# Performance work log

Measured on AMD Instinct MI355X. Metric: run time of the kernel, lower is better.

The kernel has to match this reference:

```python
import jax, jax.numpy as jnp
from jax import lax
import numpy as np

WR = 7    # window resolution
NH = 4    # attention heads
FF = 3.0  # focusing factor


def _conv_bn(x, w, s, b, groups=1):
    # Conv2d (no bias) + inference BatchNorm folded to per-channel scale/bias
    y = lax.conv_general_dilated(x, w, (1, 1), 'SAME',
        dimension_numbers=('NCHW', 'OIHW', 'NCHW'), feature_group_count=groups)
    return y * s[None, :, None, None] + b[None, :, None, None]


def _ffn(x, w1, s1, b1, w2, s2, b2):
    return _conv_bn(jax.nn.relu(_conv_bn(x, w1, s1, b1)), w2, s2, b2)


def _focus(t):
    n0 = jnp.linalg.norm(t, axis=-1, keepdims=True)
    tp = t ** FF
    return tp / jnp.linalg.norm(tp, axis=-1, keepdims=True) * n0


def _attn(xw, wq, wkv, pos, scale_p, dwc_w, dwc_b, proj_w, proj_b):
    # xw: [Bw, N=49, C] focused linear attention within one window
    Bw, N, C = xw.shape
    hd = C // NH
    q = xw @ wq.T
    kv = xw @ wkv.T
    k, v = kv[..., :C], kv[..., C:]
    k = k + pos
    sc = jax.nn.softplus(scale_p)
    q = (jax.nn.relu(q) + 1e-6) / sc
    k = (jax.nn.relu(k) + 1e-6) / sc
    q, k = _focus(q), _focus(k)
    heads = lambda t: t.reshape(Bw, N, NH, hd).transpose(0, 2, 1, 3).reshape(Bw * NH, N, hd)
    q, k, v = heads(q), heads(k), heads(v)
    z = 1.0 / (jnp.einsum('bic,bc->bi', q, k.sum(axis=1)) + 1e-6)
    # static cost-based path choice (matches torch: i=j=N, c=d=hd)
    if N * N * (hd + hd) > hd * hd * (N + N):
        kv2 = jnp.einsum('bjc,bjd->bcd', k, v)
        y = jnp.einsum('bic,bcd,bi->bid', q, kv2, z)
    else:
        qk = jnp.einsum('bic,bjc->bij', q, k)
        y = jnp.einsum('bij,bjd,bi->bid', qk, v, z)
    # depthwise-conv feature map on v
    num = int(round(N ** 0.5))
    fm = v.reshape(-1, num, num, hd).transpose(0, 3, 1, 2)  # [Bw*NH, hd, 7, 7]
    fm = lax.conv_general_dilated(fm, dwc_w, (1, 1), 'SAME',
        dimension_numbers=('NCHW', 'OIHW', 'NCHW'), feature_group_count=hd)
    fm = fm + dwc_b[None, :, None, None]
    y = y + fm.transpose(0, 2, 3, 1).reshape(-1, N, hd)
    y = y.reshape(Bw, NH, N, hd).transpose(0, 2, 1, 3).reshape(Bw, N, C)
    return y @ proj_w.T + proj_b


def _windowed_attn(x, wq, wkv, pos, scale_p, dwc_w, dwc_b, proj_w, proj_b):
    B, C, H, W = x.shape
    xh = x.transpose(0, 2, 3, 1)  # BHWC
    pb, pr = (-H) % WR, (-W) % WR
    xh = jnp.pad(xh, ((0, 0), (0, pb), (0, pr), (0, 0)))
    pH, pW = H + pb, W + pr
    nH, nW = pH // WR, pW // WR
    xw = xh.reshape(B, nH, WR, nW, WR, C).transpose(0, 1, 3, 2, 4, 5)
    xw = xw.reshape(B * nH * nW, WR * WR, C)
    xw = _attn(xw, wq, wkv, pos, scale_p, dwc_w, dwc_b, proj_w, proj_b)
    xh = xw.reshape(B, nH, nW, WR, WR, C).transpose(0, 1, 3, 2, 4, 5).reshape(B, pH, pW, C)
    return xh[:, :H, :W].transpose(0, 3, 1, 2)


def _forward(x, dw0_w, dw0_s, dw0_b, f0_w1, f0_s1, f0_b1, f0_w2, f0_s2, f0_b2,
             wq, wkv, pos, scale_p, dwc_w, dwc_b, proj_w, proj_b,
             dw1_w, dw1_s, dw1_b, f1_w1, f1_s1, f1_b1, f1_w2, f1_s2, f1_b2):
    C = x.shape[1]
    x = x + _conv_bn(x, dw0_w, dw0_s, dw0_b, groups=C)
    x = x + _ffn(x, f0_w1, f0_s1, f0_b1, f0_w2, f0_s2, f0_b2)
    x = x + _windowed_attn(x, wq, wkv, pos, scale_p, dwc_w, dwc_b, proj_w, proj_b)
    x = x + _conv_bn(x, dw1_w, dw1_s, dw1_b, groups=C)
    x = x + _ffn(x, f1_w1, f1_s1, f1_b1, f1_w2, f1_s2, f1_b2)
    return x


def setup_inputs() -> dict:
    key = jax.random.key(0)
    ks = iter(jax.random.split(key, 32))
    rn = lambda shape, s=0.02: jax.random.normal(next(ks), shape, jnp.float32) * s
    C, H, B = 256, 64, 32
    hid, hd = 2 * C, C // NH
    d = {'x': jax.random.normal(next(ks), (B, C, H, H), jnp.float32)}
    d.update(dw0_w=rn((C, 1, 3, 3)), dw0_s=jnp.ones(C), dw0_b=jnp.zeros(C))
    d.update(f0_w1=rn((hid, C, 1, 1)), f0_s1=jnp.ones(hid), f0_b1=jnp.zeros(hid),
             f0_w2=rn((C, hid, 1, 1)), f0_s2=jnp.ones(C), f0_b2=jnp.zeros(C))
    d.update(wq=rn((C, C)), wkv=rn((2 * C, C)), pos=rn((1, WR * WR, C)),
             scale_p=rn((1, 1, C)), dwc_w=rn((hd, 1, 5, 5)), dwc_b=jnp.zeros(hd),
             proj_w=rn((C, C)), proj_b=jnp.zeros(C))
    d.update(dw1_w=rn((C, 1, 3, 3)), dw1_s=jnp.ones(C), dw1_b=jnp.zeros(C))
    d.update(f1_w1=rn((hid, C, 1, 1)), f1_s1=jnp.ones(hid), f1_b1=jnp.zeros(hid),
             f1_w2=rn((C, hid, 1, 1)), f1_s2=jnp.ones(C), f1_b2=jnp.zeros(C))
    return d


def reference(x, dw0_w, dw0_s, dw0_b, f0_w1, f0_s1, f0_b1, f0_w2, f0_s2, f0_b2,
              wq, wkv, pos, scale_p, dwc_w, dwc_b, proj_w, proj_b,
              dw1_w, dw1_s, dw1_b, f1_w1, f1_s1, f1_b1, f1_w2, f1_s2, f1_b2):
    return _forward(x, dw0_w, dw0_s, dw0_b, f0_w1, f0_s1, f0_b1, f0_w2, f0_s2, f0_b2,
                    wq, wkv, pos, scale_p, dwc_w, dwc_b, proj_w, proj_b,
                    dw1_w, dw1_s, dw1_b, f1_w1, f1_s1, f1_b1, f1_w2, f1_s2, f1_b2)
```

## Files before the change

kernel.cpp:

```cpp
#include <hip/hip_runtime.h>

typedef unsigned short u16;
typedef unsigned int u32;
typedef __attribute__((ext_vector_type(8))) short bf16x8;
typedef __attribute__((ext_vector_type(4))) float f32x4;

__device__ __forceinline__ float b2f(u16 v) { return __uint_as_float(((u32)v) << 16); }
__device__ __forceinline__ u16 f2b(float f) {
  u32 u = __float_as_uint(f);
  u32 r = (u + 0x7fffu + ((u >> 16) & 1u)) >> 16;
  return (u16)r;
}
__device__ __forceinline__ void unpack8(uint4 u, float* f) {
  f[0] = __uint_as_float(u.x << 16);
  f[1] = __uint_as_float(u.x & 0xffff0000u);
  f[2] = __uint_as_float(u.y << 16);
  f[3] = __uint_as_float(u.y & 0xffff0000u);
  f[4] = __uint_as_float(u.z << 16);
  f[5] = __uint_as_float(u.z & 0xffff0000u);
  f[6] = __uint_as_float(u.w << 16);
  f[7] = __uint_as_float(u.w & 0xffff0000u);
}
__device__ __forceinline__ uint4 pack8(const u16* o) {
  return make_uint4((u32)o[0] | ((u32)o[1] << 16), (u32)o[2] | ((u32)o[3] << 16),
                    (u32)o[4] | ((u32)o[5] << 16), (u32)o[6] | ((u32)o[7] << 16));
}
__device__ __forceinline__ bf16x8 pkbf8(float4 a, float4 b) {
  union { uint4 u; bf16x8 v; } r;
  r.u.x = (__float_as_uint(a.x) >> 16) | (__float_as_uint(a.y) & 0xffff0000u);
  r.u.y = (__float_as_uint(a.z) >> 16) | (__float_as_uint(a.w) & 0xffff0000u);
  r.u.z = (__float_as_uint(b.x) >> 16) | (__float_as_uint(b.y) & 0xffff0000u);
  r.u.w = (__float_as_uint(b.z) >> 16) | (__float_as_uint(b.w) & 0xffff0000u);
  return r.v;
}

__global__ __launch_bounds__(256, 3) void dwffn(const float* __restrict__ X, float* __restrict__ Y,
                                                const float* __restrict__ DwW, const float* __restrict__ DwS,
                                                const float* __restrict__ DwB, const float* __restrict__ W1,
                                                const float* __restrict__ S1, const float* __restrict__ B1,
                                                const float* __restrict__ W2, const float* __restrict__ S2,
                                                const float* __restrict__ B2) {
  __shared__ __align__(16) u16 X1s[32 * 256];
  __shared__ __align__(16) u16 Hs[32 * 512];
  const int tid = threadIdx.x;
  const int pix0 = blockIdx.x << 5;
  const long zbase = (long)blockIdx.y * 1048576L;
  const int h0 = pix0 >> 6, w0 = pix0 & 63;

  {
    const int px = tid & 31;
    const int cg = tid >> 5;
    const int w = w0 + px;
    const int sw = (px & 7) << 3;
    for (int it = 0; it < 8; ++it) {
      const int c0 = it * 32 + cg * 4;
      u16 o[4];
#pragma unroll
      for (int cc = 0; cc < 4; ++cc) {
        const int c = c0 + cc;
        const float* xp = X + zbase + (long)c * 4096;
        float acc = 0.f;
#pragma unroll
        for (int u = 0; u < 3; u++) {
          int hh = h0 + u - 1;
          if (hh < 0 || hh > 63) continue;
#pragma unroll
          for (int v = 0; v < 3; v++) {
            int wv2 = w + v - 1;
            if (wv2 < 0 || wv2 > 63) continue;
            acc = fmaf(DwW[c * 9 + u * 3 + v], xp[hh * 64 + wv2], acc);
          }
        }
        o[cc] = f2b(xp[h0 * 64 + w] + fmaf(DwS[c], acc, DwB[c]));
      }
      *(uint2*)&X1s[px * 256 + (c0 ^ sw)] =
          make_uint2((u32)o[0] | ((u32)o[1] << 16), (u32)o[2] | ((u32)o[3] << 16));
    }
  }
  __syncthreads();

  const int lane = tid & 63, wv = tid >> 6;
  const int l15 = lane & 15, lg = lane >> 4;

  {
    f32x4 acc1[8][2];
#pragma unroll
    for (int mt = 0; mt < 8; mt++)
#pragma unroll
      for (int nt = 0; nt < 2; nt++) acc1[mt][nt] = (f32x4){0.f, 0.f, 0.f, 0.f};
    const int hbase = wv * 128;
    for (int kst = 0; kst < 8; ++kst) {
      const int k0 = kst * 32 + lg * 8;
      bf16x8 bq[2];
#pragma unroll
      for (int nt = 0; nt < 2; nt++) {
        const int pxn = nt * 16 + l15;
        bq[nt] = *(const bf16x8*)&X1s[pxn * 256 + (k0 ^ ((pxn & 7) << 3))];
      }
#pragma unroll
      for (int mt = 0; mt < 8; mt++) {
        const float* wr = W1 + (hbase + mt * 16 + l15) * 256 + k0;
        bf16x8 af = pkbf8(*(const float4*)wr, *(const float4*)(wr + 4));
        acc1[mt][0] = __builtin_amdgcn_mfma_f32_16x16x32_bf16(af, bq[0], acc1[mt][0], 0, 0, 0);
        acc1[mt][1] = __builtin_amdgcn_mfma_f32_16x16x32_bf16(af, bq[1], acc1[mt][1], 0, 0, 0);
      }
    }
#pragma unroll
    for (int mt = 0; mt < 8; mt++) {
      const int hq = hbase + mt * 16 + lg * 4;
      const float4 s1v = *(const float4*)(S1 + hq);
      const float4 b1v = *(const float4*)(B1 + hq);
#pragma unroll
      for (int nt = 0; nt < 2; nt++) {
        const int pxn = nt * 16 + l15;
        u16 o[4];
        o[0] = f2b(fmaxf(fmaf(s1v.x, acc1[mt][nt][0], b1v.x), 0.f));
        o[1] = f2b(fmaxf(fmaf(s1v.y, acc1[mt][nt][1], b1v.y), 0.f));
        o[2] = f2b(fmaxf(fmaf(s1v.z, acc1[mt][nt][2], b1v.z), 0.f));
        o[3] = f2b(fmaxf(fmaf(s1v.w, acc1[mt][nt][3], b1v.w), 0.f));
        *(uint2*)&Hs[pxn * 512 + (hq ^ ((pxn & 7) << 3))] =
            make_uint2((u32)o[0] | ((u32)o[1] << 16), (u32)o[2] | ((u32)o[3] << 16));
      }
    }
  }
  __syncthreads();

  {
    f32x4 acc2[4][2];
#pragma unroll
    for (int mt = 0; mt < 4; mt++)
#pragma unroll
      for (int nt = 0; nt < 2; nt++) acc2[mt][nt] = (f32x4){0.f, 0.f, 0.f, 0.f};
    const int cbase = wv * 64;
    for (int kst = 0; kst < 16; ++kst) {
      const int k0 = kst * 32 + lg * 8;
      bf16x8 bq[2];
#pragma unroll
      for (int nt = 0; nt < 2; nt++) {
        const int pxn = nt * 16 + l15;
        bq[nt] = *(const bf16x8*)&Hs[pxn * 512 + (k0 ^ ((pxn & 7) << 3))];
      }
#pragma unroll
      for (int mt = 0; mt < 4; mt++) {
        const float* wr = W2 + (cbase + mt * 16 + l15) * 512 + k0;
        bf16x8 af = pkbf8(*(const float4*)wr, *(const float4*)(wr + 4));
        acc2[mt][0] = __builtin_amdgcn_mfma_f32_16x16x32_bf16(af, bq[0], acc2[mt][0], 0, 0, 0);
        acc2[mt][1] = __builtin_amdgcn_mfma_f32_16x16x32_bf16(af, bq[1], acc2[mt][1], 0, 0, 0);
      }
    }
#pragma unroll
    for (int mt = 0; mt < 4; mt++) {
      const int coq = cbase + mt * 16 + lg * 4;
      const float4 s2v = *(const float4*)(S2 + coq);
      const float4 b2v = *(const float4*)(B2 + coq);
#pragma unroll
      for (int nt = 0; nt < 2; nt++) {
        const int pxn = nt * 16 + l15;
        uint2 rv = *(const uint2*)&X1s[pxn * 256 + (coq ^ ((pxn & 7) << 3))];
        float rr0 = __uint_as_float(rv.x << 16);
        float rr1 = __uint_as_float(rv.x & 0xffff0000u);
        float rr2 = __uint_as_float(rv.y << 16);
        float rr3 = __uint_as_float(rv.y & 0xffff0000u);
        float* yp = Y + zbase + (long)coq * 4096 + pix0 + pxn;
        yp[0] = fmaf(s2v.x, acc2[mt][nt][0], b2v.x) + rr0;
        yp[4096] = fmaf(s2v.y, acc2[mt][nt][1], b2v.y) + rr1;
        yp[8192] = fmaf(s2v.z, acc2[mt][nt][2], b2v.z) + rr2;
        yp[12288] = fmaf(s2v.w, acc2[mt][nt][3], b2v.w) + rr3;
      }
    }
  }
}

#define NTOK 49
#define AOFF_XW 0
#define AOFF_SQB 32768
#define AOFF_SKB 65536
#define AOFF_SVT 98304
#define AOFF_SDW 131072
#define AOFF_SSC 137728
#define AOFF_SZ 138752
#define SMEM_BYTES 139776

__global__ __launch_bounds__(512) void attn_kernel(const float* __restrict__ X, const float* __restrict__ Wq,
                                                   const float* __restrict__ Wkv, const float* __restrict__ Pos,
                                                   const float* __restrict__ ScaleP, const float* __restrict__ DwcW,
                                                   const float* __restrict__ DwcB, const float* __restrict__ PrW,
                                                   const float* __restrict__ PrB, float* __restrict__ Y) {
  extern __shared__ char smem[];
  u16* XW = (u16*)(smem + AOFF_XW);
  u16* QKB = (u16*)(smem + AOFF_XW);
  u16* SQB = (u16*)(smem + AOFF_SQB);
  u16* AO = (u16*)(smem + AOFF_SQB);
  u16* SKB = (u16*)(smem + AOFF_SKB);
  u16* SVT = (u16*)(smem + AOFF_SVT);
  float* SDW = (float*)(smem + AOFF_SDW);
  float* SSC = (float*)(smem + AOFF_SSC);
  float* SZ = (float*)(smem + AOFF_SZ);

  const int tid = threadIdx.x;
  const int wi = blockIdx.x;
  const int b = wi / 100;
  const int rem = wi - b * 100;
  const int wh = rem / 10, ww = rem - (rem / 10) * 10;
  const long bbase = (long)b * (256L * 4096L);

  if (tid < 256) SSC[tid] = log1pf(expf(ScaleP[tid]));
  for (int i = tid; i < 1600; i += 512) SDW[i] = DwcW[i];
  if (tid < 64) SDW[1600 + tid] = DwcB[tid];

  {
    const uint4 z4 = make_uint4(0, 0, 0, 0);
    uint4* zb = (uint4*)(smem + AOFF_SQB);
    for (int e = tid; e < 6144; e += 512) zb[e] = z4;
  }

  for (int u = tid; u < 64 * 32; u += 512) {
    const int cg = u >> 6, t = u & 63;
    const int c0 = cg << 3;
    u16 o[8] = {0, 0, 0, 0, 0, 0, 0, 0};
    if (t < NTOK) {
      const int r = t / 7, cc = t - r * 7;
      const int gh = wh * 7 + r, gw = ww * 7 + cc;
      if (gh < 64 && gw < 64) {
        const float* xp = X + bbase + gh * 64 + gw;
#pragma unroll
        for (int e = 0; e < 8; e++) o[e] = f2b(xp[(long)(c0 + e) * 4096]);
      }
    }
    *(uint4*)&XW[t * 256 + (c0 ^ ((t & 7) << 3))] = pack8(o);
  }
  __syncthreads();

  const int lane = tid & 63, wvid = tid >> 6;
  const int l15 = lane & 15, lg = lane >> 4;

  {
    const float* wr_base[6];
    int tile[6];
#pragma unroll
    for (int mt = 0; mt < 6; mt++) {
      const int tl = wvid + (mt << 3);
      tile[mt] = tl;
      const int row = (tl << 4) + l15;
      wr_base[mt] = (row < 256) ? (Wq + row * 256) : (Wkv + (row - 256) * 256);
    }
    f32x4 acc[6][4];
#pragma unroll
    for (int mt = 0; mt < 6; mt++)
#pragma unroll
      for (int nt = 0; nt < 4; nt++) acc[mt][nt] = (f32x4){0.f, 0.f, 0.f, 0.f};
    for (int kst = 0; kst < 8; ++kst) {
      const int k0 = kst * 32 + lg * 8;
      bf16x8 bq[4];
#pragma unroll
      for (int nt = 0; nt < 4; nt++) {
        const int tkn = (nt << 4) + l15;
        bq[nt] = *(const bf16x8*)&XW[tkn * 256 + (k0 ^ ((tkn & 7) << 3))];
      }
#pragma unroll
      for (int mt = 0; mt < 6; mt++) {
        bf16x8 af = pkbf8(*(const float4*)(wr_base[mt] + k0), *(const float4*)(wr_base[mt] + k0 + 4));
#pragma unroll
        for (int nt = 0; nt < 4; nt++)
          acc[mt][nt] = __builtin_amdgcn_mfma_f32_16x16x32_bf16(af, bq[nt], acc[mt][nt], 0, 0, 0);
      }
    }
#pragma unroll
    for (int mt = 0; mt < 6; mt++) {
      const int tl = tile[mt];
#pragma unroll
      for (int nt = 0; nt < 4; nt++) {
        const int tkn = (nt << 4) + l15;
        if (tkn >= NTOK) continue;
        const int sw = (tkn & 7) << 3;
        if (tl < 16) {
          const int jq = (tl << 4) + (lg << 2);
          const float4 sc = *(const float4*)(SSC + jq);
          u16 o[4];
          o[0] = f2b((fmaxf(acc[mt][nt][0], 0.f) + 1e-6f) / sc.x);
          o[1] = f2b((fmaxf(acc[mt][nt][1], 0.f) + 1e-6f) / sc.y);
          o[2] = f2b((fmaxf(acc[mt][nt][2], 0.f) + 1e-6f) / sc.z);
          o[3] = f2b((fmaxf(acc[mt][nt][3], 0.f) + 1e-6f) / sc.w);
          *(uint2*)&SQB[tkn * 256 + (jq ^ sw)] = make_uint2((u32)o[0] | ((u32)o[1] << 16), (u32)o[2] | ((u32)o[3] << 16));
        } else if (tl < 32) {
          const int kc = ((tl - 16) << 4) + (lg << 2);
          const float4 sc = *(const float4*)(SSC + kc);
          const float4 pp = *(const float4*)(Pos + tkn * 256 + kc);
          u16 o[4];
          o[0] = f2b((fmaxf(acc[mt][nt][0] + pp.x, 0.f) + 1e-6f) / sc.x);
          o[1] = f2b((fmaxf(acc[mt][nt][1] + pp.y, 0.f) + 1e-6f) / sc.y);
          o[2] = f2b((fmaxf(acc[mt][nt][2] + pp.z, 0.f) + 1e-6f) / sc.z);
          o[3] = f2b((fmaxf(acc[mt][nt][3] + pp.w, 0.f) + 1e-6f) / sc.w);
          *(uint2*)&SKB[tkn * 256 + (kc ^ sw)] = make_uint2((u32)o[0] | ((u32)o[1] << 16), (u32)o[2] | ((u32)o[3] << 16));
        } else {
          const int vc = ((tl - 32) << 4) + (lg << 2);
#pragma unroll
          for (int cc = 0; cc < 4; cc++) {
            const int d = vc + cc;
            SVT[d * 64 + (tkn ^ ((d & 7) << 3))] = f2b(acc[mt][nt][cc]);
          }
        }
      }
    }
  }
  __syncthreads();

  for (int t = wvid; t < NTOK; t += 8) {
    const int sw = (t & 7) << 3;
    float qv[4], ss = 0.f, s6 = 0.f;
#pragma unroll
    for (int m = 0; m < 4; m++) {
      float v = b2f(SQB[t * 256 + ((lane + (m << 6)) ^ sw)]);
      qv[m] = v;
      ss += v * v;
      float c3 = v * v * v;
      s6 += c3 * c3;
    }
#pragma unroll
    for (int off = 1; off < 64; off <<= 1) {
      ss += __shfl_xor(ss, off, 64);
      s6 += __shfl_xor(s6, off, 64);
    }
    float scl = sqrtf(ss) / sqrtf(s6);
#pragma unroll
    for (int m = 0; m < 4; m++) {
      float v = qv[m];
      SQB[t * 256 + ((lane + (m << 6)) ^ sw)] = f2b(v * v * v * scl);
    }
    float kv[4];
    ss = 0.f;
    s6 = 0.f;
#pragma unroll
    for (int m = 0; m < 4; m++) {
      float v = b2f(SKB[t * 256 + ((lane + (m << 6)) ^ sw)]);
      kv[m] = v;
      ss += v * v;
      float c3 = v * v * v;
      s6 += c3 * c3;
    }
#pragma unroll
    for (int off = 1; off < 64; off <<= 1) {
      ss += __shfl_xor(ss, off, 64);
      s6 += __shfl_xor(s6, off, 64);
    }
    scl = sqrtf(ss) / sqrtf(s6);
#pragma unroll
    for (int m = 0; m < 4; m++) {
      float v = kv[m];
      SKB[t * 256 + ((lane + (m << 6)) ^ sw)] = f2b(v * v * v * scl);
    }
  }
  __syncthreads();

  for (int jj = 0; jj < 8; ++jj) {
    const int job = (jj << 3) + wvid;
    const int h = job >> 4;
    const int r2 = job & 15;
    const int ti = r2 >> 2, tj = r2 & 3;
    const int hb = h << 6;
    f32x4 a = (f32x4){0.f, 0.f, 0.f, 0.f};
#pragma unroll
    for (int kst = 0; kst < 2; ++kst) {
      const int k0 = hb + kst * 32 + lg * 8;
      const int irow = ti * 16 + l15;
      const int jrow = tj * 16 + l15;
      bf16x8 qa = *(const bf16x8*)&SQB[irow * 256 + (k0 ^ ((irow & 7) << 3))];
      bf16x8 kb = *(const bf16x8*)&SKB[jrow * 256 + (k0 ^ ((jrow & 7) << 3))];
      a = __builtin_amdgcn_mfma_f32_16x16x32_bf16(qa, kb, a, 0, 0, 0);
    }
#pragma unroll
    for (int reg = 0; reg < 4; ++reg) {
      const int i = ti * 16 + lg * 4 + reg, j = tj * 16 + l15;
      QKB[((h << 6) + i) * 64 + (j ^ ((i & 7) << 3))] = f2b(a[reg]);
    }
  }
  __syncthreads();

  if (tid < 256) {
    const uint4* rowp = (const uint4*)&QKB[tid * 64];
    float s = 0.f;
#pragma unroll
    for (int k = 0; k < 8; k++) {
      uint4 uu = rowp[(k + tid) & 7];
      float f[8];
      unpack8(uu, f);
#pragma unroll
      for (int e = 0; e < 8; e++) s += f[e];
    }
    SZ[tid] = 1.f / (s + 1e-6f);
  }
  __syncthreads();

  for (int jj = 0; jj < 8; ++jj) {
    const int job = (jj << 3) + wvid;
    const int ti = job >> 4;
    const int dt = job & 15;
    const int h = dt >> 2;
    f32x4 a = (f32x4){0.f, 0.f, 0.f, 0.f};
#pragma unroll
    for (int kst = 0; kst < 2; ++kst) {
      const int j0 = kst * 32 + lg * 8;
      const int irow = ti * 16 + l15;
      const int drow = (dt << 4) + l15;
      bf16x8 qk = *(const bf16x8*)&QKB[((h << 6) + irow) * 64 + (j0 ^ ((irow & 7) << 3))];
      bf16x8 vt = *(const bf16x8*)&SVT[drow * 64 + (j0 ^ ((drow & 7) << 3))];
      a = __builtin_amdgcn_mfma_f32_16x16x32_bf16(qk, vt, a, 0, 0, 0);
    }
#pragma unroll
    for (int reg = 0; reg < 4; ++reg) {
      const int i = ti * 16 + lg * 4 + reg;
      const int d = (dt << 4) + l15;
      const float z = SZ[(h << 6) + i];
      AO[i * 256 + (d ^ ((i & 7) << 3))] = f2b(a[reg] * z);
    }
  }
  __syncthreads();

  {
    const int d = tid >> 1, half = tid & 1;
    const int dch = d & 63;
    const float bias = SDW[1600 + dch];
    const int swd = (d & 7) << 3;
    const u16* vrow = SVT + d * 64;
    const float* wrow = SDW + dch * 25;
    const int rlo = half ? 4 : 0, rhi = half ? 7 : 4;
    for (int r = rlo; r < rhi; ++r) {
      for (int c = 0; c < 7; ++c) {
        float fm = bias;
#pragma unroll
        for (int u = 0; u < 5; u++) {
          const int rr = r + u - 2;
          if (rr < 0 || rr > 6) continue;
#pragma unroll
          for (int v = 0; v < 5; v++) {
            const int cc = c + v - 2;
            if (cc < 0 || cc > 6) continue;
            fm = fmaf(b2f(vrow[(rr * 7 + cc) ^ swd]), wrow[u * 5 + v], fm);
          }
        }
        const int t = r * 7 + c;
        const int idx = t * 256 + (d ^ ((t & 7) << 3));
        AO[idx] = f2b(b2f(AO[idx]) + fm);
      }
    }
  }
  __syncthreads();

  {
    f32x4 acc[2][4];
#pragma unroll
    for (int mt = 0; mt < 2; mt++)
#pragma unroll
      for (int nt = 0; nt < 4; nt++) acc[mt][nt] = (f32x4){0.f, 0.f, 0.f, 0.f};
    const int cbase = wvid * 32;
    for (int kst = 0; kst < 8; ++kst) {
      const int k0 = kst * 32 + lg * 8;
      bf16x8 bq[4];
#pragma unroll
      for (int nt = 0; nt < 4; nt++) {
        const int tkn = (nt << 4) + l15;
        bq[nt] = *(const bf16x8*)&AO[tkn * 256 + (k0 ^ ((tkn & 7) << 3))];
      }
#pragma unroll
      for (int mt = 0; mt < 2; mt++) {
        const float* wr = PrW + (cbase + mt * 16 + l15) * 256 + k0;
        bf16x8 af = pkbf8(*(const float4*)wr, *(const float4*)(wr + 4));
#pragma unroll
        for (int nt = 0; nt < 4; nt++)
          acc[mt][nt] = __builtin_amdgcn_mfma_f32_16x16x32_bf16(af, bq[nt], acc[mt][nt], 0, 0, 0);
      }
    }
#pragma unroll
    for (int mt = 0; mt < 2; mt++) {
      const int coq = cbase + mt * 16 + (lg << 2);
      const float4 pbv = *(const float4*)(PrB + coq);
#pragma unroll
      for (int nt = 0; nt < 4; nt++) {
        const int tkn = (nt << 4) + l15;
        if (tkn >= NTOK) continue;
        const int r = tkn / 7, cc = tkn - r * 7;
        const int gh = wh * 7 + r, gw = ww * 7 + cc;
        if (gh < 64 && gw < 64) {
          const long addr = bbase + (long)coq * 4096 + gh * 64 + gw;
          Y[addr] = acc[mt][nt][0] + pbv.x + X[addr];
          Y[addr + 4096] = acc[mt][nt][1] + pbv.y + X[addr + 4096];
          Y[addr + 8192] = acc[mt][nt][2] + pbv.z + X[addr + 8192];
          Y[addr + 12288] = acc[mt][nt][3] + pbv.w + X[addr + 12288];
        }
      }
    }
  }
}

extern "C" void kernel_launch(void* const* d_in, const int* in_sizes, int n_in, void* d_out, int out_size,
                              void* d_ws, size_t ws_size, hipStream_t stream) {
  const float* x = (const float*)d_in[0];
  const float* dw0_w = (const float*)d_in[1];
  const float* dw0_s = (const float*)d_in[2];
  const float* dw0_b = (const float*)d_in[3];
  const float* f0_w1 = (const float*)d_in[4];
  const float* f0_s1 = (const float*)d_in[5];
  const float* f0_b1 = (const float*)d_in[6];
  const float* f0_w2 = (const float*)d_in[7];
  const float* f0_s2 = (const float*)d_in[8];
  const float* f0_b2 = (const float*)d_in[9];
  const float* wq = (const float*)d_in[10];
  const float* wkv = (const float*)d_in[11];
  const float* pos = (const float*)d_in[12];
  const float* scale_p = (const float*)d_in[13];
  const float* dwc_w = (const float*)d_in[14];
  const float* dwc_b = (const float*)d_in[15];
  const float* proj_w = (const float*)d_in[16];
  const float* proj_b = (const float*)d_in[17];
  const float* dw1_w = (const float*)d_in[18];
  const float* dw1_s = (const float*)d_in[19];
  const float* dw1_b = (const float*)d_in[20];
  const float* f1_w1 = (const float*)d_in[21];
  const float* f1_s1 = (const float*)d_in[22];
  const float* f1_b1 = (const float*)d_in[23];
  const float* f1_w2 = (const float*)d_in[24];
  const float* f1_s2 = (const float*)d_in[25];
  const float* f1_b2 = (const float*)d_in[26];

  float* D = (float*)d_out;
  const size_t nbytes = (size_t)out_size * sizeof(float);
  float* A = (ws_size >= nbytes) ? (float*)d_ws : (float*)d_in[0];

  (void)hipFuncSetAttribute((const void*)attn_kernel, hipFuncAttributeMaxDynamicSharedMemorySize, SMEM_BYTES);

  dwffn<<<dim3(128, 32), 256, 0, stream>>>(x, D, dw0_w, dw0_s, dw0_b, f0_w1, f0_s1, f0_b1, f0_w2, f0_s2, f0_b2);
  attn_kernel<<<3200, 512, SMEM_BYTES, stream>>>(D, wq, wkv, pos, scale_p, dwc_w, dwc_b, proj_w, proj_b, A);
  dwffn<<<dim3(128, 32), 256, 0, stream>>>(A, D, dw1_w, dw1_s, dw1_b, f1_w1, f1_s1, f1_b1, f1_w2, f1_s2, f1_b2);
}
```

Measured before the change: 2.957 ms.

## Double threads per block in dwffn and attention kernels

Both the depthwise+FFN kernel and the windowed attention kernel now launch twice as many threads per block (512 and 1024). Each wave handles half as many MFMA row tiles, with tiles interleaved across waves, and the loops over tokens, jobs and conv rows are re-strided to match. The aim is more waves per block to hide the latency of global weight loads and conversions, and fewer accumulator registers per thread. The cost is that each weight row is still fetched per wave, synchronisation now spans more waves, and the 1024-thread attention blocks with large shared memory may limit occupancy.

```diff
diff --git a/kernel.cpp b/kernel.cpp
--- a/kernel.cpp
+++ b/kernel.cpp
@@ -34,7 +34,7 @@
   return r.v;
 }
 
-__global__ __launch_bounds__(256, 3) void dwffn(const float* __restrict__ X, float* __restrict__ Y,
+__global__ __launch_bounds__(512, 4) void dwffn(const float* __restrict__ X, float* __restrict__ Y,
                                                 const float* __restrict__ DwW, const float* __restrict__ DwS,
                                                 const float* __restrict__ DwB, const float* __restrict__ W1,
                                                 const float* __restrict__ S1, const float* __restrict__ B1,
@@ -52,8 +52,8 @@
     const int cg = tid >> 5;
     const int w = w0 + px;
     const int sw = (px & 7) << 3;
-    for (int it = 0; it < 8; ++it) {
-      const int c0 = it * 32 + cg * 4;
+    for (int it = 0; it < 4; ++it) {
+      const int c0 = it * 64 + cg * 4;
       u16 o[4];
 #pragma unroll
       for (int cc = 0; cc < 4; ++cc) {
@@ -83,12 +83,11 @@
   const int l15 = lane & 15, lg = lane >> 4;
 
   {
-    f32x4 acc1[8][2];
-#pragma unroll
-    for (int mt = 0; mt < 8; mt++)
+    f32x4 acc1[4][2];
+#pragma unroll
+    for (int mt = 0; mt < 4; mt++)
 #pragma unroll
       for (int nt = 0; nt < 2; nt++) acc1[mt][nt] = (f32x4){0.f, 0.f, 0.f, 0.f};
-    const int hbase = wv * 128;
     for (int kst = 0; kst < 8; ++kst) {
       const int k0 = kst * 32 + lg * 8;
       bf16x8 bq[2];
@@ -98,16 +97,17 @@
         bq[nt] = *(const bf16x8*)&X1s[pxn * 256 + (k0 ^ ((pxn & 7) << 3))];
       }
 #pragma unroll
-      for (int mt = 0; mt < 8; mt++) {
-        const float* wr = W1 + (hbase + mt * 16 + l15) * 256 + k0;
+      for (int mt = 0; mt < 4; mt++) {
+        const int hrow = ((wv + (mt << 3)) << 4) + l15;
+        const float* wr = W1 + hrow * 256 + k0;
         bf16x8 af = pkbf8(*(const float4*)wr, *(const float4*)(wr + 4));
         acc1[mt][0] = __builtin_amdgcn_mfma_f32_16x16x32_bf16(af, bq[0], acc1[mt][0], 0, 0, 0);
         acc1[mt][1] = __builtin_amdgcn_mfma_f32_16x16x32_bf16(af, bq[1], acc1[mt][1], 0, 0, 0);
       }
     }
 #pragma unroll
-    for (int mt = 0; mt < 8; mt++) {
-      const int hq = hbase + mt * 16 + lg * 4;
+    for (int mt = 0; mt < 4; mt++) {
+      const int hq = ((wv + (mt << 3)) << 4) + lg * 4;
       const float4 s1v = *(const float4*)(S1 + hq);
       const float4 b1v = *(const float4*)(B1 + hq);
 #pragma unroll
@@ -126,12 +126,11 @@
   __syncthreads();
 
   {
-    f32x4 acc2[4][2];
-#pragma unroll
-    for (int mt = 0; mt < 4; mt++)
+    f32x4 acc2[2][2];
+#pragma unroll
+    for (int mt = 0; mt < 2; mt++)
 #pragma unroll
       for (int nt = 0; nt < 2; nt++) acc2[mt][nt] = (f32x4){0.f, 0.f, 0.f, 0.f};
-    const int cbase = wv * 64;
     for (int kst = 0; kst < 16; ++kst) {
       const int k0 = kst * 32 + lg * 8;
       bf16x8 bq[2];
@@ -141,16 +140,17 @@
         bq[nt] = *(const bf16x8*)&Hs[pxn * 512 + (k0 ^ ((pxn & 7) << 3))];
       }
 #pragma unroll
-      for (int mt = 0; mt < 4; mt++) {
-        const float* wr = W2 + (cbase + mt * 16 + l15) * 512 + k0;
+      for (int mt = 0; mt < 2; mt++) {
+        const int crow = ((wv + (mt << 3)) << 4) + l15;
+        const float* wr = W2 + crow * 512 + k0;
         bf16x8 af = pkbf8(*(const float4*)wr, *(const float4*)(wr + 4));
         acc2[mt][0] = __builtin_amdgcn_mfma_f32_16x16x32_bf16(af, bq[0], acc2[mt][0], 0, 0, 0);
         acc2[mt][1] = __builtin_amdgcn_mfma_f32_16x16x32_bf16(af, bq[1], acc2[mt][1], 0, 0, 0);
       }
     }
 #pragma unroll
-    for (int mt = 0; mt < 4; mt++) {
-      const int coq = cbase + mt * 16 + lg * 4;
+    for (int mt = 0; mt < 2; mt++) {
+      const int coq = ((wv + (mt << 3)) << 4) + lg * 4;
       const float4 s2v = *(const float4*)(S2 + coq);
       const float4 b2v = *(const float4*)(B2 + coq);
 #pragma unroll
@@ -181,11 +181,11 @@
 #define AOFF_SZ 138752
 #define SMEM_BYTES 139776
 
-__global__ __launch_bounds__(512) void attn_kernel(const float* __restrict__ X, const float* __restrict__ Wq,
-                                                   const float* __restrict__ Wkv, const float* __restrict__ Pos,
-                                                   const float* __restrict__ ScaleP, const float* __restrict__ DwcW,
-                                                   const float* __restrict__ DwcB, const float* __restrict__ PrW,
-                                                   const float* __restrict__ PrB, float* __restrict__ Y) {
+__global__ __launch_bounds__(1024) void attn_kernel(const float* __restrict__ X, const float* __restrict__ Wq,
+                                                    const float* __restrict__ Wkv, const float* __restrict__ Pos,
+                                                    const float* __restrict__ ScaleP, const float* __restrict__ DwcW,
+                                                    const float* __restrict__ DwcB, const float* __restrict__ PrW,
+                                                    const float* __restrict__ PrB, float* __restrict__ Y) {
   extern __shared__ char smem[];
   u16* XW = (u16*)(smem + AOFF_XW);
   u16* QKB = (u16*)(smem + AOFF_XW);
@@ -205,16 +205,16 @@
   const long bbase = (long)b * (256L * 4096L);
 
   if (tid < 256) SSC[tid] = log1pf(expf(ScaleP[tid]));
-  for (int i = tid; i < 1600; i += 512) SDW[i] = DwcW[i];
+  for (int i = tid; i < 1600; i += 1024) SDW[i] = DwcW[i];
   if (tid < 64) SDW[1600 + tid] = DwcB[tid];
 
   {
     const uint4 z4 = make_uint4(0, 0, 0, 0);
     uint4* zb = (uint4*)(smem + AOFF_SQB);
-    for (int e = tid; e < 6144; e += 512) zb[e] = z4;
-  }
-
-  for (int u = tid; u < 64 * 32; u += 512) {
+    for (int e = tid; e < 6144; e += 1024) zb[e] = z4;
+  }
+
+  for (int u = tid; u < 64 * 32; u += 1024) {
     const int cg = u >> 6, t = u & 63;
     const int c0 = cg << 3;
     u16 o[8] = {0, 0, 0, 0, 0, 0, 0, 0};
@@ -235,18 +235,18 @@
   const int l15 = lane & 15, lg = lane >> 4;
 
   {
-    const float* wr_base[6];
-    int tile[6];
-#pragma unroll
-    for (int mt = 0; mt < 6; mt++) {
-      const int tl = wvid + (mt << 3);
+    const float* wr_base[3];
+    int tile[3];
+#pragma unroll
+    for (int mt = 0; mt < 3; mt++) {
+      const int tl = wvid + (mt << 4);
       tile[mt] = tl;
       const int row = (tl << 4) + l15;
       wr_base[mt] = (row < 256) ? (Wq + row * 256) : (Wkv + (row - 256) * 256);
     }
-    f32x4 acc[6][4];
-#pragma unroll
-    for (int mt = 0; mt < 6; mt++)
+    f32x4 acc[3][4];
+#pragma unroll
+    for (int mt = 0; mt < 3; mt++)
 #pragma unroll
       for (int nt = 0; nt < 4; nt++) acc[mt][nt] = (f32x4){0.f, 0.f, 0.f, 0.f};
     for (int kst = 0; kst < 8; ++kst) {
@@ -258,7 +258,7 @@
         bq[nt] = *(const bf16x8*)&XW[tkn * 256 + (k0 ^ ((tkn & 7) << 3))];
       }
 #pragma unroll
-      for (int mt = 0; mt < 6; mt++) {
+      for (int mt = 0; mt < 3; mt++) {
         bf16x8 af = pkbf8(*(const float4*)(wr_base[mt] + k0), *(const float4*)(wr_base[mt] + k0 + 4));
 #pragma unroll
         for (int nt = 0; nt < 4; nt++)
@@ -266,7 +266,7 @@
       }
     }
 #pragma unroll
-    for (int mt = 0; mt < 6; mt++) {
+    for (int mt = 0; mt < 3; mt++) {
       const int tl = tile[mt];
 #pragma unroll
       for (int nt = 0; nt < 4; nt++) {
@@ -305,7 +305,7 @@
   }
   __syncthreads();
 
-  for (int t = wvid; t < NTOK; t += 8) {
+  for (int t = wvid; t < NTOK; t += 16) {
     const int sw = (t & 7) << 3;
     float qv[4], ss = 0.f, s6 = 0.f;
 #pragma unroll
@@ -352,8 +352,8 @@
   }
   __syncthreads();
 
-  for (int jj = 0; jj < 8; ++jj) {
-    const int job = (jj << 3) + wvid;
+  for (int jj = 0; jj < 4; ++jj) {
+    const int job = (jj << 4) + wvid;
     const int h = job >> 4;
     const int r2 = job & 15;
     const int ti = r2 >> 2, tj = r2 & 3;
@@ -391,8 +391,8 @@
   }
   __syncthreads();
 
-  for (int jj = 0; jj < 8; ++jj) {
-    const int job = (jj << 3) + wvid;
+  for (int jj = 0; jj < 4; ++jj) {
+    const int job = (jj << 4) + wvid;
     const int ti = job >> 4;
     const int dt = job & 15;
     const int h = dt >> 2;
@@ -417,13 +417,14 @@
   __syncthreads();
 
   {
-    const int d = tid >> 1, half = tid & 1;
+    const int d = tid >> 2;
+    const int q4 = tid & 3;
     const int dch = d & 63;
     const float bias = SDW[1600 + dch];
     const int swd = (d & 7) << 3;
     const u16* vrow = SVT + d * 64;
     const float* wrow = SDW + dch * 25;
-    const int rlo = half ? 4 : 0, rhi = half ? 7 : 4;
+    const int rlo = q4 * 2, rhi = (q4 == 3) ? 7 : (q4 * 2 + 2);
     for (int r = rlo; r < rhi; ++r) {
       for (int c = 0; c < 7; ++c) {
         float fm = bias;
@@ -447,12 +448,10 @@
   __syncthreads();
 
   {
-    f32x4 acc[2][4];
-#pragma unroll
-    for (int mt = 0; mt < 2; mt++)
-#pragma unroll
-      for (int nt = 0; nt < 4; nt++) acc[mt][nt] = (f32x4){0.f, 0.f, 0.f, 0.f};
-    const int cbase = wvid * 32;
+    f32x4 acc[4];
+#pragma unroll
+    for (int nt = 0; nt < 4; nt++) acc[nt] = (f32x4){0.f, 0.f, 0.f, 0.f};
+    const int cbase = wvid << 4;
     for (int kst = 0; kst < 8; ++kst) {
       const int k0 = kst * 32 + lg * 8;
       bf16x8 bq[4];
@@ -461,32 +460,26 @@
         const int tkn = (nt << 4) + l15;
         bq[nt] = *(const bf16x8*)&AO[tkn * 256 + (k0 ^ ((tkn & 7) << 3))];
       }
-#pragma unroll
-      for (int mt = 0; mt < 2; mt++) {
-        const float* wr = PrW + (cbase + mt * 16 + l15) * 256 + k0;
-        bf16x8 af = pkbf8(*(const float4*)wr, *(const float4*)(wr + 4));
-#pragma unroll
-        for (int nt = 0; nt < 4; nt++)
-          acc[mt][nt] = __builtin_amdgcn_mfma_f32_16x16x32_bf16(af, bq[nt], acc[mt][nt], 0, 0, 0);
-      }
-    }
-#pragma unroll
-    for (int mt = 0; mt < 2; mt++) {
-      const int coq = cbase + mt * 16 + (lg << 2);
-      const float4 pbv = *(const float4*)(PrB + coq);
-#pragma unroll
-      for (int nt = 0; nt < 4; nt++) {
-        const int tkn = (nt << 4) + l15;
-        if (tkn >= NTOK) continue;
-        const int r = tkn / 7, cc = tkn - r * 7;
-        const int gh = wh * 7 + r, gw = ww * 7 + cc;
-        if (gh < 64 && gw < 64) {
-          const long addr = bbase + (long)coq * 4096 + gh * 64 + gw;
-          Y[addr] = acc[mt][nt][0] + pbv.x + X[addr];
-          Y[addr + 4096] = acc[mt][nt][1] + pbv.y + X[addr + 4096];
-          Y[addr + 8192] = acc[mt][nt][2] + pbv.z + X[addr + 8192];
-          Y[addr + 12288] = acc[mt][nt][3] + pbv.w + X[addr + 12288];
-        }
+      const float* wr = PrW + (cbase + l15) * 256 + k0;
+      bf16x8 af = pkbf8(*(const float4*)wr, *(const float4*)(wr + 4));
+#pragma unroll
+      for (int nt = 0; nt < 4; nt++)
+        acc[nt] = __builtin_amdgcn_mfma_f32_16x16x32_bf16(af, bq[nt], acc[nt], 0, 0, 0);
+    }
+    const int coq = cbase + (lg << 2);
+    const float4 pbv = *(const float4*)(PrB + coq);
+#pragma unroll
+    for (int nt = 0; nt < 4; nt++) {
+      const int tkn = (nt << 4) + l15;
+      if (tkn >= NTOK) continue;
+      const int r = tkn / 7, cc = tkn - r * 7;
+      const int gh = wh * 7 + r, gw = ww * 7 + cc;
+      if (gh < 64 && gw < 64) {
+        const long addr = bbase + (long)coq * 4096 + gh * 64 + gw;
+        Y[addr] = acc[nt][0] + pbv.x + X[addr];
+        Y[addr + 4096] = acc[nt][1] + pbv.y + X[addr + 4096];
+        Y[addr + 8192] = acc[nt][2] + pbv.z + X[addr + 8192];
+        Y[addr + 12288] = acc[nt][3] + pbv.w + X[addr + 12288];
       }
     }
   }
@@ -528,7 +521,7 @@
 
   (void)hipFuncSetAttribute((const void*)attn_kernel, hipFuncAttributeMaxDynamicSharedMemorySize, SMEM_BYTES);
 
-  dwffn<<<dim3(128, 32), 256, 0, stream>>>(x, D, dw0_w, dw0_s, dw0_b, f0_w1, f0_s1, f0_b1, f0_w2, f0_s2, f0_b2);
-  attn_kernel<<<3200, 512, SMEM_BYTES, stream>>>(D, wq, wkv, pos, scale_p, dwc_w, dwc_b, proj_w, proj_b, A);
-  dwffn<<<dim3(128, 32), 256, 0, stream>>>(A, D, dw1_w, dw1_s, dw1_b, f1_w1, f1_s1, f1_b1, f1_w2, f1_s2, f1_b2);
-}
+  dwffn<<<dim3(128, 32), 512, 0, stream>>>(x, D, dw0_w, dw0_s, dw0_b, f0_w1, f0_s1, f0_b1, f0_w2, f0_s2, f0_b2);
+  attn_kernel<<<3200, 1024, SMEM_BYTES, stream>>>(D, wq, wkv, pos, scale_p, dwc_w, dwc_b, proj_w, proj_b, A);
+  dwffn<<<dim3(128, 32), 512, 0, stream>>>(A, D, dw1_w, dw1_s, dw1_b, f1_w1, f1_s1, f1_b1, f1_w2, f1_s2, f1_b2);
+}
```

After: 2.615 ms. 11.6% less time.
